# Kernel tuning notes

Hardware: AMD Instinct MI355X
Metric: run time of the kernel (lower is better)

Reference implementation:

```python
import jax, jax.numpy as jnp
import numpy as np

D_MODEL = 2048
NUM_HEADS = 16
D_K = D_MODEL // NUM_HEADS
THETA = 10000.0
MAX_SEQ_LEN = 2048
GPT_INIT_STD = 0.02


def setup_inputs() -> dict:
    key = jax.random.key(0)
    ks = jax.random.split(key, 5)
    B, T = 4, 2048
    x = jax.random.normal(ks[0], (B, T, D_MODEL), dtype=jnp.float32)
    token_positions = jnp.arange(T, dtype=jnp.int64 if jax.config.jax_enable_x64 else jnp.int32)[None, :]
    Wq = jax.random.normal(ks[1], (D_MODEL, D_MODEL), dtype=jnp.float32) * GPT_INIT_STD
    Wk = jax.random.normal(ks[2], (D_MODEL, D_MODEL), dtype=jnp.float32) * GPT_INIT_STD
    Wv = jax.random.normal(ks[3], (D_MODEL, D_MODEL), dtype=jnp.float32) * GPT_INIT_STD
    Wo = jax.random.normal(ks[4], (D_MODEL, D_MODEL), dtype=jnp.float32) * GPT_INIT_STD
    return {"x": x, "token_positions": token_positions, "Wq": Wq, "Wk": Wk, "Wv": Wv, "Wo": Wo}


def _rope_tables(dtype):
    # angles[p, j] = p * theta^(-2j/d_k), j in [0, d_k/2)
    j = jnp.arange(D_K // 2, dtype=jnp.float32)
    inv_freq = THETA ** (-2.0 * j / float(D_K))
    pos = jnp.arange(MAX_SEQ_LEN, dtype=jnp.float32)[:, None]
    angles = pos * inv_freq[None, :]
    return jnp.cos(angles).astype(dtype), jnp.sin(angles).astype(dtype)


def _apply_rope(t, cos_pos, sin_pos):
    # t: (b, h, s, d); cos/sin: (1, s, d/2) -> broadcast over (b, h)
    even = t[..., 0::2]
    odd = t[..., 1::2]
    c = cos_pos[:, None, :, :]  # (1,1,s,d/2)
    s = sin_pos[:, None, :, :]
    rot_even = even * c - odd * s
    rot_odd = even * s + odd * c
    out = jnp.stack([rot_even, rot_odd], axis=-1)  # (b,h,s,d/2,2)
    return out.reshape(t.shape)


def reference(x, token_positions, Wq, Wk, Wv, Wo):
    B, T, D = x.shape
    H, d = NUM_HEADS, D_K
    q = (x @ Wq.T).reshape(B, T, H, d).transpose(0, 2, 1, 3)  # (b,h,t,d)
    k = (x @ Wk.T).reshape(B, T, H, d).transpose(0, 2, 1, 3)
    v = (x @ Wv.T).reshape(B, T, H, d).transpose(0, 2, 1, 3)

    cos_tab, sin_tab = _rope_tables(x.dtype)
    cos_pos = cos_tab[token_positions]  # (1, t, d/2)
    sin_pos = sin_tab[token_positions]
    q = _apply_rope(q, cos_pos, sin_pos)
    k = _apply_rope(k, cos_pos, sin_pos)

    # token_positions is strictly increasing and attention_mask is None,
    # so build_attention_mask returns None -> unmasked eager attention.
    scale = float(d) ** -0.5
    scores = jnp.einsum('bhtd,bhsd->bhts', q, k) * scale
    attn = jax.nn.softmax(scores.astype(jnp.float32), axis=-1).astype(q.dtype)
    out = jnp.einsum('bhts,bhsd->bhtd', attn, v)  # (b,h,t,d)
    out = out.transpose(0, 2, 1, 3).reshape(B, T, D)  # (b,t,h*d)
    return out @ Wo.T
```

## Files before the change

kernel.cpp:

```cpp
#include <hip/hip_runtime.h>
#include <hip/hip_bf16.h>
#include <math.h>

#define TSEQ   2048
#define DMODEL 2048
#define NHEAD  16
#define DHEAD  128
#define NBATCH 4
#define MROWS  (NBATCH*TSEQ)

typedef __attribute__((ext_vector_type(8))) short v8s;
typedef __attribute__((ext_vector_type(4))) short v4s;
typedef __attribute__((ext_vector_type(4))) float v4f;
typedef __attribute__((ext_vector_type(16))) float v16f;

#if __has_builtin(__builtin_amdgcn_exp2f)
#define EXP2(x) __builtin_amdgcn_exp2f(x)
#else
#define EXP2(x) __expf((x) * 0.6931471805599453f)
#endif

__device__ __forceinline__ unsigned short f2b(float f) {
  __hip_bfloat16 h = __float2bfloat16(f);
  return *reinterpret_cast<unsigned short*>(&h);
}
__device__ __forceinline__ unsigned int cvtpk(float lo, float hi) {
  unsigned int r;
  asm("v_cvt_pk_bf16_f32 %0, %1, %2" : "=v"(r) : "v"(lo), "v"(hi));
  return r;
}
__device__ __forceinline__ void gload_lds16(const unsigned short* g, unsigned short* l) {
  __builtin_amdgcn_global_load_lds(
      (const __attribute__((address_space(1))) unsigned int*)g,
      (__attribute__((address_space(3))) unsigned int*)l, 16, 0, 0);
}

__global__ void prep_kernel(const float* __restrict__ x,  const float* __restrict__ Wq,
                            const float* __restrict__ Wk, const float* __restrict__ Wv,
                            const float* __restrict__ Wo, const int* __restrict__ pos,
                            unsigned short* __restrict__ xb,  unsigned short* __restrict__ wqb,
                            unsigned short* __restrict__ wkb, unsigned short* __restrict__ wvb,
                            unsigned short* __restrict__ wob,
                            float* __restrict__ cosT, float* __restrict__ sinT) {
  const int blk = blockIdx.x, tid = threadIdx.x;
  if (blk < 32768) {
    const float* in; unsigned short* out; int lb;
    if      (blk < 16384) { in = x;  out = xb;  lb = blk; }
    else if (blk < 20480) { in = Wq; out = wqb; lb = blk - 16384; }
    else if (blk < 24576) { in = Wk; out = wkb; lb = blk - 20480; }
    else if (blk < 28672) { in = Wv; out = wvb; lb = blk - 24576; }
    else                  { in = Wo; out = wob; lb = blk - 28672; }
    int i = lb * 256 + tid;
    float4 v = reinterpret_cast<const float4*>(in)[i];
    ushort4 o;
    o.x = f2b(v.x); o.y = f2b(v.y); o.z = f2b(v.z); o.w = f2b(v.w);
    reinterpret_cast<ushort4*>(out)[i] = o;
  } else {
    int idx = (blk - 32768) * 256 + tid;
    int t = idx >> 6, j = idx & 63;
    float p = (float)pos[t];
    float inv_freq = expf((-2.0f * (float)j / 128.0f) * logf(10000.0f));
    float ang = p * inv_freq;
    cosT[idx] = cosf(ang);
    sinT[idx] = sinf(ang);
  }
}

template<int MODE>
__global__ __launch_bounds__(512, 2) void gemm8(const unsigned short* __restrict__ A,
                                                const unsigned short* __restrict__ Bt,
                                                void* __restrict__ Cout,
                                                void* __restrict__ CoutK,
                                                const float* __restrict__ cosT,
                                                const float* __restrict__ sinT) {
  __shared__ unsigned short ldsA[2][256 * 64];
  __shared__ unsigned short ldsB[2][256 * 64];
  const int tid = threadIdx.x;
  const int lane = tid & 63, wv = tid >> 6;
  const int wr = wv >> 2, wc = wv & 3;
  const int g = lane >> 4, r16 = lane & 15;
  const int r7 = r16 & 7;
  const int sl0 = (g ^ r7) << 3;
  const int sl1 = ((4 + g) ^ r7) << 3;

  const int nx = gridDim.x;
  const int nwg = nx * gridDim.y;
  const int lid = blockIdx.y * nx + blockIdx.x;
  const int q8 = nwg >> 3, r8 = nwg & 7;
  const int xcd = lid & 7, off = lid >> 3;
  const int nlid = (xcd < r8 ? xcd * (q8 + 1) : r8 * (q8 + 1) + (xcd - r8) * q8) + off;
  const int mrow0 = (nlid / nx) * 256;
  const int ncol0 = (nlid % nx) * 256;

  const int srow = tid >> 3;
  const int sslot = tid & 7;

  auto stA = [&](int kt, int b, int hf) {
    const int k0 = kt * 64;
#pragma unroll
    for (int j = 0; j < 2; ++j) {
      int r = hf * 128 + j * 64 + srow;
      int slot = sslot ^ (r & 7);
      gload_lds16(&A[(size_t)(mrow0 + r) * DMODEL + k0 + slot * 8],
                  &ldsA[b][(hf * 128 + j * 64) * 64 + tid * 8]);
    }
  };
  auto stB = [&](int kt, int b, int hf) {
    const int k0 = kt * 64;
#pragma unroll
    for (int j = 0; j < 2; ++j) {
      int r = hf * 128 + j * 64 + srow;
      int slot = sslot ^ (r & 7);
      gload_lds16(&Bt[(size_t)(ncol0 + r) * DMODEL + k0 + slot * 8],
                  &ldsB[b][(hf * 128 + j * 64) * 64 + tid * 8]);
    }
  };

  v4f zero = {0.f, 0.f, 0.f, 0.f};
  v4f acc[8][4];
#pragma unroll
  for (int m = 0; m < 8; ++m)
#pragma unroll
    for (int n = 0; n < 4; ++n) acc[m][n] = zero;

  stA(0, 0, 0); stA(0, 0, 1); stB(0, 0, 0); stB(0, 0, 1);
  stA(1, 1, 0); stA(1, 1, 1); stB(1, 1, 0); stB(1, 1, 1);
  asm volatile("s_waitcnt vmcnt(8)" ::: "memory");
  __builtin_amdgcn_s_barrier();

  v8s af[4][2], bf[4][2];
  const int arow = wr * 128 + r16;
  const int brow = wc * 64 + r16;

  for (int kt = 0; kt < DMODEL / 64; ++kt) {
    const int p = kt & 1;
    unsigned short* LA = ldsA[p];
    unsigned short* LB = ldsB[p];

#pragma unroll
    for (int m = 0; m < 4; ++m) {
      af[m][0] = *(const v8s*)&LA[(arow + m * 16) * 64 + sl0];
      af[m][1] = *(const v8s*)&LA[(arow + m * 16) * 64 + sl1];
    }
#pragma unroll
    for (int n = 0; n < 2; ++n) {
      bf[n][0] = *(const v8s*)&LB[(brow + n * 16) * 64 + sl0];
      bf[n][1] = *(const v8s*)&LB[(brow + n * 16) * 64 + sl1];
    }
    __builtin_amdgcn_s_barrier();
    asm volatile("s_waitcnt lgkmcnt(0)" ::: "memory");
    __builtin_amdgcn_sched_barrier(0);
    __builtin_amdgcn_s_setprio(1);
#pragma unroll
    for (int m = 0; m < 4; ++m)
#pragma unroll
      for (int n = 0; n < 2; ++n) {
        acc[m][n] = __builtin_amdgcn_mfma_f32_16x16x32_bf16(af[m][0], bf[n][0], acc[m][n], 0, 0, 0);
        acc[m][n] = __builtin_amdgcn_mfma_f32_16x16x32_bf16(af[m][1], bf[n][1], acc[m][n], 0, 0, 0);
      }
    __builtin_amdgcn_s_setprio(0);
    __builtin_amdgcn_s_barrier();

#pragma unroll
    for (int n = 2; n < 4; ++n) {
      bf[n][0] = *(const v8s*)&LB[(brow + n * 16) * 64 + sl0];
      bf[n][1] = *(const v8s*)&LB[(brow + n * 16) * 64 + sl1];
    }
    __builtin_amdgcn_s_barrier();
    asm volatile("s_waitcnt lgkmcnt(0)" ::: "memory");
    __builtin_amdgcn_sched_barrier(0);
    __builtin_amdgcn_s_setprio(1);
#pragma unroll
    for (int m = 0; m < 4; ++m)
#pragma unroll
      for (int n = 2; n < 4; ++n) {
        acc[m][n] = __builtin_amdgcn_mfma_f32_16x16x32_bf16(af[m][0], bf[n][0], acc[m][n], 0, 0, 0);
        acc[m][n] = __builtin_amdgcn_mfma_f32_16x16x32_bf16(af[m][1], bf[n][1], acc[m][n], 0, 0, 0);
      }
    __builtin_amdgcn_s_setprio(0);
    __builtin_amdgcn_s_barrier();

#pragma unroll
    for (int m = 0; m < 4; ++m) {
      af[m][0] = *(const v8s*)&LA[(arow + 64 + m * 16) * 64 + sl0];
      af[m][1] = *(const v8s*)&LA[(arow + 64 + m * 16) * 64 + sl1];
    }
    if (kt < DMODEL / 64 - 2) { stB(kt + 2, p, 0); stB(kt + 2, p, 1); }
    __builtin_amdgcn_s_barrier();
    asm volatile("s_waitcnt lgkmcnt(0)" ::: "memory");
    __builtin_amdgcn_sched_barrier(0);
    __builtin_amdgcn_s_setprio(1);
#pragma unroll
    for (int m = 0; m < 4; ++m)
#pragma unroll
      for (int n = 2; n < 4; ++n) {
        acc[m + 4][n] = __builtin_amdgcn_mfma_f32_16x16x32_bf16(af[m][0], bf[n][0], acc[m + 4][n], 0, 0, 0);
        acc[m + 4][n] = __builtin_amdgcn_mfma_f32_16x16x32_bf16(af[m][1], bf[n][1], acc[m + 4][n], 0, 0, 0);
      }
    __builtin_amdgcn_s_setprio(0);
    __builtin_amdgcn_s_barrier();

    if (kt < DMODEL / 64 - 2) {
      stA(kt + 2, p, 0); stA(kt + 2, p, 1);
      asm volatile("s_waitcnt vmcnt(8)" ::: "memory");
    } else {
      asm volatile("s_waitcnt vmcnt(0)" ::: "memory");
    }
    __builtin_amdgcn_s_barrier();
    __builtin_amdgcn_s_setprio(1);
#pragma unroll
    for (int m = 0; m < 4; ++m)
#pragma unroll
      for (int n = 0; n < 2; ++n) {
        acc[m + 4][n] = __builtin_amdgcn_mfma_f32_16x16x32_bf16(af[m][0], bf[n][0], acc[m + 4][n], 0, 0, 0);
        acc[m + 4][n] = __builtin_amdgcn_mfma_f32_16x16x32_bf16(af[m][1], bf[n][1], acc[m + 4][n], 0, 0, 0);
      }
    __builtin_amdgcn_s_setprio(0);
    __builtin_amdgcn_s_barrier();
  }

#pragma unroll
  for (int m = 0; m < 8; ++m) {
#pragma unroll
    for (int n = 0; n < 4; ++n) {
#pragma unroll
      for (int r = 0; r < 4; ++r) {
        int row = mrow0 + wr * 128 + m * 16 + g * 4 + r;
        int col = ncol0 + wc * 64 + n * 16 + r16;
        float val = acc[m][n][r];
        if (MODE == 0) {
          int t = row & (TSEQ - 1), bb = row >> 11;
          int isK = col >> 11;
          int hh = (col >> 7) & (NHEAD - 1), dd = col & (DHEAD - 1);
          float c = cosT[(t << 6) + (dd >> 1)];
          float s = sinT[(t << 6) + (dd >> 1)];
          float pv = __shfl_xor(val, 1);
          float rot = (r16 & 1) ? (pv * s + val * c) : (val * c - pv * s);
          if (!isK) rot *= 0.12751726f;
          unsigned short* dst = (unsigned short*)(isK ? CoutK : Cout);
          dst[(((size_t)bb * NHEAD + hh) * TSEQ + t) * DHEAD + dd] = f2b(rot);
        } else if (MODE == 2) {
          int hh = row >> 7, dd = row & (DHEAD - 1);
          int bb = col >> 11, tt = col & (TSEQ - 1);
          ((unsigned short*)Cout)[(((size_t)bb * NHEAD + hh) * DHEAD + dd) * TSEQ + tt] = f2b(val);
        } else {
          ((float*)Cout)[(size_t)row * DMODEL + col] = val;
        }
      }
    }
  }
}

__global__ __launch_bounds__(256, 2) void attn_kernel(const unsigned short* __restrict__ Q,
                                                      const unsigned short* __restrict__ K,
                                                      const unsigned short* __restrict__ Vt,
                                                      unsigned short* __restrict__ O) {
  __shared__ unsigned short Ks[64 * 128];
  __shared__ unsigned short Vs[128 * 64];
  const int tid = threadIdx.x, lane = tid & 63, w = tid >> 6;
  const int hi = lane >> 5, l31 = lane & 31;
  const int bh = blockIdx.y;
  const int b = bh >> 4, h = bh & 15;
  const int qbase = blockIdx.x * 128;
  const size_t hb = (size_t)bh * TSEQ * DHEAD;
  const size_t vb = (size_t)bh * DHEAD * TSEQ;

  v8s qf[8];
  {
    const int qrow = qbase + w * 32 + l31;
#pragma unroll
    for (int dk = 0; dk < 8; ++dk)
      qf[dk] = *(const v8s*)&Q[hb + (size_t)qrow * DHEAD + dk * 16 + hi * 8];
  }

  v16f Z16 = {0,0,0,0,0,0,0,0,0,0,0,0,0,0,0,0};
  v16f o_acc[4];
#pragma unroll
  for (int d = 0; d < 4; ++d) o_acc[d] = Z16;
  float l_run = 0.0f;

  const int ck0 = tid;
  v8s kst[4], vst[4];

#pragma unroll
  for (int hh = 0; hh < 4; ++hh) {
    int ck = ck0 + hh * 256;
    kst[hh] = *(const v8s*)&K[hb + (size_t)(ck >> 4) * DHEAD + (ck & 15) * 8];
    vst[hh] = *(const v8s*)&Vt[vb + (size_t)(ck >> 3) * TSEQ + (ck & 7) * 8];
  }
#pragma unroll
  for (int hh = 0; hh < 4; ++hh) {
    int ck = ck0 + hh * 256;
    int kr = ck >> 4, kc = (ck & 15) * 8;
    *(v8s*)&Ks[kr * 128 + (kc ^ ((kr & 15) << 3))] = kst[hh];
    int vr = ck >> 3, vc = (ck & 7) * 8;
    int g0 = (((vc >> 2)    ) ^ (vr & 15)) << 2;
    int g1 = (((vc >> 2) + 1) ^ (vr & 15)) << 2;
    union { v8s v; v4s hf[2]; } uu; uu.v = vst[hh];
    *(v4s*)&Vs[vr * 64 + g0] = uu.hf[0];
    *(v4s*)&Vs[vr * 64 + g1] = uu.hf[1];
  }
  __syncthreads();

  for (int s0 = 0; s0 < TSEQ; s0 += 64) {
    const bool last = (s0 + 64 >= TSEQ);
    if (!last) {
#pragma unroll
      for (int hh = 0; hh < 4; ++hh) {
        int ck = ck0 + hh * 256;
        kst[hh] = *(const v8s*)&K[hb + (size_t)(s0 + 64 + (ck >> 4)) * DHEAD + (ck & 15) * 8];
      }
#pragma unroll
      for (int hh = 0; hh < 4; ++hh) {
        int ck = ck0 + hh * 256;
        vst[hh] = *(const v8s*)&Vt[vb + (size_t)(ck >> 3) * TSEQ + s0 + 64 + (ck & 7) * 8];
      }
    }

    v16f s[2]; s[0] = Z16; s[1] = Z16;
    __builtin_amdgcn_s_setprio(1);
#pragma unroll
    for (int kvt = 0; kvt < 2; ++kvt) {
#pragma unroll
      for (int dk = 0; dk < 8; ++dk) {
        int krow = kvt * 32 + l31;
        v8s a = *(const v8s*)&Ks[krow * 128 + ((dk * 16 + hi * 8) ^ ((krow & 15) << 3))];
        s[kvt] = __builtin_amdgcn_mfma_f32_32x32x16_bf16(a, qf[dk], s[kvt], 0, 0, 0);
      }
    }
    __builtin_amdgcn_s_setprio(0);

    __syncthreads();

    if (!last) {
#pragma unroll
      for (int hh = 0; hh < 4; ++hh) {
        int ck = ck0 + hh * 256;
        int kr = ck >> 4, kc = (ck & 15) * 8;
        *(v8s*)&Ks[kr * 128 + (kc ^ ((kr & 15) << 3))] = kst[hh];
      }
    }

    float rowsum = 0.f;
#pragma unroll
    for (int kvt = 0; kvt < 2; ++kvt)
#pragma unroll
      for (int r = 0; r < 16; ++r) {
        float pp = EXP2(s[kvt][r]);
        s[kvt][r] = pp; rowsum += pp;
      }
    l_run += rowsum + __shfl_xor(rowsum, 32);

#pragma unroll
    for (int kvt = 0; kvt < 2; ++kvt) {
      unsigned int wpk[8];
#pragma unroll
      for (int i = 0; i < 8; ++i) wpk[i] = cvtpk(s[kvt][2 * i], s[kvt][2 * i + 1]);
      asm("v_permlane32_swap_b32 %0, %1" : "+v"(wpk[0]), "+v"(wpk[2]));
      asm("v_permlane32_swap_b32 %0, %1" : "+v"(wpk[1]), "+v"(wpk[3]));
      asm("v_permlane32_swap_b32 %0, %1" : "+v"(wpk[4]), "+v"(wpk[6]));
      asm("v_permlane32_swap_b32 %0, %1" : "+v"(wpk[5]), "+v"(wpk[7]));
      union { unsigned int u[4]; v8s v; } pa, pb;
      pa.u[0] = wpk[0]; pa.u[1] = wpk[1]; pa.u[2] = wpk[2]; pa.u[3] = wpk[3];
      pb.u[0] = wpk[4]; pb.u[1] = wpk[5]; pb.u[2] = wpk[6]; pb.u[3] = wpk[7];

      const int c0 = kvt * 32 + hi * 8;
      __builtin_amdgcn_s_setprio(1);
#pragma unroll
      for (int d = 0; d < 4; ++d) {
        int drow = d * 32 + l31;
        int sw = (drow & 15) << 2;
        union { v4s hf[2]; v8s v; } vf0, vf1;
        vf0.hf[0] = *(const v4s*)&Vs[drow * 64 + ((c0     ) ^ sw)];
        vf0.hf[1] = *(const v4s*)&Vs[drow * 64 + ((c0 +  4) ^ sw)];
        vf1.hf[0] = *(const v4s*)&Vs[drow * 64 + ((c0 + 16) ^ sw)];
        vf1.hf[1] = *(const v4s*)&Vs[drow * 64 + ((c0 + 20) ^ sw)];
        o_acc[d] = __builtin_amdgcn_mfma_f32_32x32x16_bf16(pa.v, vf0.v, o_acc[d], 0, 0, 0);
        o_acc[d] = __builtin_amdgcn_mfma_f32_32x32x16_bf16(pb.v, vf1.v, o_acc[d], 0, 0, 0);
      }
      __builtin_amdgcn_s_setprio(0);
    }

    __syncthreads();

    if (!last) {
#pragma unroll
      for (int hh = 0; hh < 4; ++hh) {
        int ck = ck0 + hh * 256;
        int vr = ck >> 3, vc = (ck & 7) * 8;
        int g0 = (((vc >> 2)    ) ^ (vr & 15)) << 2;
        int g1 = (((vc >> 2) + 1) ^ (vr & 15)) << 2;
        union { v8s v; v4s hf[2]; } uu; uu.v = vst[hh];
        *(v4s*)&Vs[vr * 64 + g0] = uu.hf[0];
        *(v4s*)&Vs[vr * 64 + g1] = uu.hf[1];
      }
    }
  }

#pragma unroll
  for (int r = 0; r < 16; ++r) {
    int qi = (r & 3) + 8 * (r >> 2) + 4 * hi;
    float lq = __shfl(l_run, qi);
    float inv = 1.0f / lq;
    int t = qbase + w * 32 + qi;
#pragma unroll
    for (int d = 0; d < 4; ++d) {
      O[((size_t)(b * TSEQ + t)) * DMODEL + h * DHEAD + d * 32 + l31] = f2b(o_acc[d][r] * inv);
    }
  }
}

extern "C" void kernel_launch(void* const* d_in, const int* in_sizes, int n_in,
                              void* d_out, int out_size, void* d_ws, size_t ws_size,
                              hipStream_t stream) {
  const float* x  = (const float*)d_in[0];
  const int*   pos = (const int*)d_in[1];
  const float* Wq = (const float*)d_in[2];
  const float* Wk = (const float*)d_in[3];
  const float* Wv = (const float*)d_in[4];
  const float* Wo = (const float*)d_in[5];
  float* out = (float*)d_out;
  char* ws = (char*)d_ws;

  const size_t WBYTES = (size_t)DMODEL * DMODEL * 2;
  const size_t XBYTES = (size_t)MROWS * DMODEL * 2;
  unsigned short* wqb = (unsigned short*)(ws);
  unsigned short* wkb = (unsigned short*)(ws + WBYTES);
  unsigned short* wvb = (unsigned short*)(ws + 2 * WBYTES);
  unsigned short* wob = (unsigned short*)(ws + 3 * WBYTES);
  unsigned short* xb  = (unsigned short*)(ws + 4 * WBYTES);
  unsigned short* Qb  = (unsigned short*)(ws + 4 * WBYTES + XBYTES);
  unsigned short* Kb  = (unsigned short*)(ws + 4 * WBYTES + 2 * XBYTES);
  unsigned short* Vtb = (unsigned short*)(ws + 4 * WBYTES + 3 * XBYTES);
  float* cosT = (float*)(ws + 4 * WBYTES + 4 * XBYTES);
  float* sinT = cosT + TSEQ * 64;
  if (ws_size < 4 * WBYTES + 4 * XBYTES + 2 * (size_t)TSEQ * 64 * sizeof(float)) return;

  prep_kernel<<<33280, 256, 0, stream>>>(x, Wq, Wk, Wv, Wo, pos,
                                         xb, wqb, wkb, wvb, wob, cosT, sinT);

  gemm8<0><<<dim3(2 * DMODEL / 256, MROWS / 256), 512, 0, stream>>>(
      xb, wqb, (void*)Qb, (void*)Kb, cosT, sinT);
  gemm8<2><<<dim3(MROWS / 256, DMODEL / 256), 512, 0, stream>>>(
      wvb, xb, (void*)Vtb, nullptr, cosT, sinT);

  attn_kernel<<<dim3(TSEQ / 128, 64), 256, 0, stream>>>(Qb, Kb, Vtb, xb);

  gemm8<3><<<dim3(DMODEL / 256, MROWS / 256), 512, 0, stream>>>(
      xb, wob, (void*)out, nullptr, cosT, sinT);
}
```

Measured before the change: 495.6 us.

## Widen V LDS swizzle to 8-element reads and split fused QK projection GEMM

The attention kernel now stores V tiles in LDS with an 8-element-granular XOR swizzle, so each PV operand takes one 128-bit LDS read instead of two 64-bit reads. The P fragments for both KV sub-tiles are packed before the MFMA loop, which runs under a single priority raise. The per-iteration cross-half rowsum shuffle is moved to a single combine in the epilogue. Separately, the fused Q|K projection GEMM is split into two launches (MODE 0 and MODE 1), which drops the per-element Q/K branch in the epilogue but adds a launch and halves the blocks per launch.

Measured after the change: 485.1 us. 2.1% less time.

```diff
diff --git a/kernel.cpp b/kernel.cpp
--- a/kernel.cpp
+++ b/kernel.cpp
@@ -10,7 +10,6 @@
 #define MROWS  (NBATCH*TSEQ)
 
 typedef __attribute__((ext_vector_type(8))) short v8s;
-typedef __attribute__((ext_vector_type(4))) short v4s;
 typedef __attribute__((ext_vector_type(4))) float v4f;
 typedef __attribute__((ext_vector_type(16))) float v16f;
 
@@ -70,7 +69,6 @@
 __global__ __launch_bounds__(512, 2) void gemm8(const unsigned short* __restrict__ A,
                                                 const unsigned short* __restrict__ Bt,
                                                 void* __restrict__ Cout,
-                                                void* __restrict__ CoutK,
                                                 const float* __restrict__ cosT,
                                                 const float* __restrict__ sinT) {
   __shared__ unsigned short ldsA[2][256 * 64];
@@ -228,17 +226,15 @@
         int row = mrow0 + wr * 128 + m * 16 + g * 4 + r;
         int col = ncol0 + wc * 64 + n * 16 + r16;
         float val = acc[m][n][r];
-        if (MODE == 0) {
+        if (MODE <= 1) {
           int t = row & (TSEQ - 1), bb = row >> 11;
-          int isK = col >> 11;
-          int hh = (col >> 7) & (NHEAD - 1), dd = col & (DHEAD - 1);
+          int hh = col >> 7, dd = col & (DHEAD - 1);
           float c = cosT[(t << 6) + (dd >> 1)];
           float s = sinT[(t << 6) + (dd >> 1)];
           float pv = __shfl_xor(val, 1);
           float rot = (r16 & 1) ? (pv * s + val * c) : (val * c - pv * s);
-          if (!isK) rot *= 0.12751726f;
-          unsigned short* dst = (unsigned short*)(isK ? CoutK : Cout);
-          dst[(((size_t)bb * NHEAD + hh) * TSEQ + t) * DHEAD + dd] = f2b(rot);
+          if (MODE == 0) rot *= 0.12751726f;
+          ((unsigned short*)Cout)[(((size_t)bb * NHEAD + hh) * TSEQ + t) * DHEAD + dd] = f2b(rot);
         } else if (MODE == 2) {
           int hh = row >> 7, dd = row & (DHEAD - 1);
           int bb = col >> 11, tt = col & (TSEQ - 1);
@@ -293,12 +289,8 @@
     int ck = ck0 + hh * 256;
     int kr = ck >> 4, kc = (ck & 15) * 8;
     *(v8s*)&Ks[kr * 128 + (kc ^ ((kr & 15) << 3))] = kst[hh];
-    int vr = ck >> 3, vc = (ck & 7) * 8;
-    int g0 = (((vc >> 2)    ) ^ (vr & 15)) << 2;
-    int g1 = (((vc >> 2) + 1) ^ (vr & 15)) << 2;
-    union { v8s v; v4s hf[2]; } uu; uu.v = vst[hh];
-    *(v4s*)&Vs[vr * 64 + g0] = uu.hf[0];
-    *(v4s*)&Vs[vr * 64 + g1] = uu.hf[1];
+    int vr = ck >> 3, vg = ck & 7;
+    *(v8s*)&Vs[vr * 64 + (((vg ^ (vr & 7))) << 3)] = vst[hh];
   }
   __syncthreads();
 
@@ -349,8 +341,9 @@
         float pp = EXP2(s[kvt][r]);
         s[kvt][r] = pp; rowsum += pp;
       }
-    l_run += rowsum + __shfl_xor(rowsum, 32);
-
+    l_run += rowsum;
+
+    union { unsigned int u[4]; v8s v; } pf[4];
 #pragma unroll
     for (int kvt = 0; kvt < 2; ++kvt) {
       unsigned int wpk[8];
@@ -360,26 +353,27 @@
       asm("v_permlane32_swap_b32 %0, %1" : "+v"(wpk[1]), "+v"(wpk[3]));
       asm("v_permlane32_swap_b32 %0, %1" : "+v"(wpk[4]), "+v"(wpk[6]));
       asm("v_permlane32_swap_b32 %0, %1" : "+v"(wpk[5]), "+v"(wpk[7]));
-      union { unsigned int u[4]; v8s v; } pa, pb;
-      pa.u[0] = wpk[0]; pa.u[1] = wpk[1]; pa.u[2] = wpk[2]; pa.u[3] = wpk[3];
-      pb.u[0] = wpk[4]; pb.u[1] = wpk[5]; pb.u[2] = wpk[6]; pb.u[3] = wpk[7];
-
-      const int c0 = kvt * 32 + hi * 8;
-      __builtin_amdgcn_s_setprio(1);
+      pf[2 * kvt].u[0] = wpk[0]; pf[2 * kvt].u[1] = wpk[1];
+      pf[2 * kvt].u[2] = wpk[2]; pf[2 * kvt].u[3] = wpk[3];
+      pf[2 * kvt + 1].u[0] = wpk[4]; pf[2 * kvt + 1].u[1] = wpk[5];
+      pf[2 * kvt + 1].u[2] = wpk[6]; pf[2 * kvt + 1].u[3] = wpk[7];
+    }
+
+    __builtin_amdgcn_s_setprio(1);
+#pragma unroll
+    for (int kvt = 0; kvt < 2; ++kvt) {
+      const int g0 = kvt * 4 + hi;
 #pragma unroll
       for (int d = 0; d < 4; ++d) {
         int drow = d * 32 + l31;
-        int sw = (drow & 15) << 2;
-        union { v4s hf[2]; v8s v; } vf0, vf1;
-        vf0.hf[0] = *(const v4s*)&Vs[drow * 64 + ((c0     ) ^ sw)];
-        vf0.hf[1] = *(const v4s*)&Vs[drow * 64 + ((c0 +  4) ^ sw)];
-        vf1.hf[0] = *(const v4s*)&Vs[drow * 64 + ((c0 + 16) ^ sw)];
-        vf1.hf[1] = *(const v4s*)&Vs[drow * 64 + ((c0 + 20) ^ sw)];
-        o_acc[d] = __builtin_amdgcn_mfma_f32_32x32x16_bf16(pa.v, vf0.v, o_acc[d], 0, 0, 0);
-        o_acc[d] = __builtin_amdgcn_mfma_f32_32x32x16_bf16(pb.v, vf1.v, o_acc[d], 0, 0, 0);
-      }
-      __builtin_amdgcn_s_setprio(0);
-    }
+        int sx = drow & 7;
+        v8s vf0 = *(const v8s*)&Vs[drow * 64 + (((g0    ) ^ sx) << 3)];
+        v8s vf1 = *(const v8s*)&Vs[drow * 64 + (((g0 + 2) ^ sx) << 3)];
+        o_acc[d] = __builtin_amdgcn_mfma_f32_32x32x16_bf16(pf[2 * kvt].v, vf0, o_acc[d], 0, 0, 0);
+        o_acc[d] = __builtin_amdgcn_mfma_f32_32x32x16_bf16(pf[2 * kvt + 1].v, vf1, o_acc[d], 0, 0, 0);
+      }
+    }
+    __builtin_amdgcn_s_setprio(0);
 
     __syncthreads();
 
@@ -387,12 +381,8 @@
 #pragma unroll
       for (int hh = 0; hh < 4; ++hh) {
         int ck = ck0 + hh * 256;
-        int vr = ck >> 3, vc = (ck & 7) * 8;
-        int g0 = (((vc >> 2)    ) ^ (vr & 15)) << 2;
-        int g1 = (((vc >> 2) + 1) ^ (vr & 15)) << 2;
-        union { v8s v; v4s hf[2]; } uu; uu.v = vst[hh];
-        *(v4s*)&Vs[vr * 64 + g0] = uu.hf[0];
-        *(v4s*)&Vs[vr * 64 + g1] = uu.hf[1];
+        int vr = ck >> 3, vg = ck & 7;
+        *(v8s*)&Vs[vr * 64 + (((vg ^ (vr & 7))) << 3)] = vst[hh];
       }
     }
   }
@@ -400,7 +390,7 @@
 #pragma unroll
   for (int r = 0; r < 16; ++r) {
     int qi = (r & 3) + 8 * (r >> 2) + 4 * hi;
-    float lq = __shfl(l_run, qi);
+    float lq = __shfl(l_run, qi) + __shfl(l_run, qi + 32);
     float inv = 1.0f / lq;
     int t = qbase + w * 32 + qi;
 #pragma unroll
@@ -439,13 +429,12 @@
   prep_kernel<<<33280, 256, 0, stream>>>(x, Wq, Wk, Wv, Wo, pos,
                                          xb, wqb, wkb, wvb, wob, cosT, sinT);
 
-  gemm8<0><<<dim3(2 * DMODEL / 256, MROWS / 256), 512, 0, stream>>>(
-      xb, wqb, (void*)Qb, (void*)Kb, cosT, sinT);
-  gemm8<2><<<dim3(MROWS / 256, DMODEL / 256), 512, 0, stream>>>(
-      wvb, xb, (void*)Vtb, nullptr, cosT, sinT);
+  dim3 gg(DMODEL / 256, MROWS / 256);
+  gemm8<0><<<gg, 512, 0, stream>>>(xb, wqb, (void*)Qb, cosT, sinT);
+  gemm8<1><<<gg, 512, 0, stream>>>(xb, wkb, (void*)Kb, cosT, sinT);
+  gemm8<2><<<dim3(MROWS / 256, DMODEL / 256), 512, 0, stream>>>(wvb, xb, (void*)Vtb, cosT, sinT);
 
   attn_kernel<<<dim3(TSEQ / 128, 64), 256, 0, stream>>>(Qb, Kb, Vtb, xb);
 
-  gemm8<3><<<dim3(DMODEL / 256, MROWS / 256), 512, 0, stream>>>(
-      xb, wob, (void*)out, nullptr, cosT, sinT);
-}
+  gemm8<3><<<gg, 512, 0, stream>>>(xb, wob, (void*)out, cosT, sinT);
+}
```
